# Kernel optimization log

Hardware: AMD Instinct MI355X
Metric: run time of the kernel (lower is better)

The kernel has to match this reference:

```python
import jax, jax.numpy as jnp
import numpy as np

TEMPERATURE = 0.05
BETA = 1.0
LAMBDA_THRESHOLD = 0.7


def setup_inputs() -> dict:
    key = jax.random.key(0)
    k1, k2 = jax.random.split(key)
    B, D = 8192, 256
    features = jax.random.normal(k1, (B, D), dtype=jnp.float32)
    labels = jax.random.randint(k2, (B,), 0, 100, dtype=jnp.int64)
    return {"features": features, "labels": labels}


def reference(features, labels):
    B = features.shape[0]
    eps = 1e-12
    # L2 normalize rows
    f = features / jnp.maximum(jnp.linalg.norm(features, axis=1, keepdims=True), eps)
    sim = jnp.matmul(f, f.T) / TEMPERATURE                      # [B, B]
    sim_max = jnp.max(sim, axis=1, keepdims=True)               # [B, 1]
    sim_stable = sim - sim_max

    same = (labels[:, None] == labels[None, :])
    eye = jnp.eye(B, dtype=bool)
    pos_mask = same & ~eye                                       # [B, B] bool

    # Denominator: logsumexp over all non-self entries per row
    exp_sim = jnp.exp(sim_stable) * (~eye)
    log_denom = jnp.log(jnp.sum(exp_sim, axis=1, keepdims=True) + eps) + sim_max  # [B,1]

    # SCL term: mean over positive pairs of (log_denom[i] - sim[i,j])
    pos_f = pos_mask.astype(sim.dtype)
    n_pos = jnp.sum(pos_f)
    scl_sum = jnp.sum(pos_f * (log_denom - sim))
    scl_loss = jnp.where(n_pos > 0, scl_sum / jnp.maximum(n_pos, 1.0), 0.0)

    # Relaxation term: per row, logsumexp over high-sim positive logits + baseline
    high = (sim * TEMPERATURE > LAMBDA_THRESHOLD) & pos_mask     # [B, B] bool
    neg_inf = jnp.asarray(-jnp.inf, sim.dtype)
    masked_logits = jnp.where(high, sim_stable, neg_inf)          # [B, B]
    baseline = (1.0 / TEMPERATURE) - sim_max                      # [B, 1]
    all_logits = jnp.concatenate([masked_logits, baseline], axis=1)  # [B, B+1]
    row_lse = jax.nn.logsumexp(all_logits, axis=1)                # [B]
    row_has = jnp.any(high, axis=1)
    n_high = jnp.sum(high.astype(sim.dtype))
    relax_sum = jnp.sum(jnp.where(row_has, row_lse, 0.0))
    relaxation_loss = jnp.where(n_high > 0, relax_sum / jnp.maximum(n_high, 1.0), 0.0)

    total = scl_loss + BETA * relaxation_loss
    return jnp.clip(total, 0.0, 10.0)
```

## Files before the change

### kernel.cpp

```cpp
#include <hip/hip_runtime.h>
#include <hip/hip_bf16.h>
#include <math.h>

#define B_N 8192
#define D_K 256
#define TILE 128
#define NT 512
#define NBLK 64
#define NPAIR 2080
#define NCLS 100
#define KEXP 28.8539008177792681f

typedef __attribute__((ext_vector_type(8))) short short8;
typedef __attribute__((ext_vector_type(4))) float f32x4;

__device__ __forceinline__ unsigned short f2bf(float x) {
    unsigned int u = __float_as_uint(x);
    unsigned int r = (u + 0x7FFFu + ((u >> 16) & 1u)) >> 16;
    return (unsigned short)r;
}

__device__ __forceinline__ void gload_lds16(const short* g, short* l) {
    __builtin_amdgcn_global_load_lds(
        (const __attribute__((address_space(1))) void*)g,
        (__attribute__((address_space(3))) void*)l, 16, 0, 0);
}

__global__ void prep_kernel(const float* __restrict__ feat, unsigned short* __restrict__ fnorm,
                            float* __restrict__ inv_norm, float* __restrict__ gscal) {
    if (blockIdx.x == 0 && threadIdx.x < 2) gscal[threadIdx.x] = 0.f;
    int wave = threadIdx.x >> 6, lane = threadIdx.x & 63;
    int row = blockIdx.x * 4 + wave;
    float4 v = *(const float4*)(feat + (size_t)row * D_K + lane * 4);
    float ss = v.x * v.x + v.y * v.y + v.z * v.z + v.w * v.w;
    #pragma unroll
    for (int off = 1; off < 64; off <<= 1) ss += __shfl_xor(ss, off);
    float inv = 1.0f / fmaxf(sqrtf(ss), 1e-12f);
    if (lane == 0) inv_norm[row] = inv;
    ushort4 o;
    o.x = f2bf(v.x * inv); o.y = f2bf(v.y * inv);
    o.z = f2bf(v.z * inv); o.w = f2bf(v.w * inv);
    *(ushort4*)(fnorm + (size_t)row * D_K + lane * 4) = o;
}

__global__ void hist_kernel(const float* __restrict__ feat, const int* __restrict__ labels,
                            const float* __restrict__ inv_norm,
                            int* __restrict__ cnt, float* __restrict__ gscal) {
    int c = blockIdx.x, tid = threadIdx.x;
    __shared__ unsigned short list[B_N];
    __shared__ int cntS;
    __shared__ float red[4];
    if (tid == 0) cntS = 0;
    __syncthreads();
    for (int r = tid; r < B_N; r += 256)
        if (labels[r] == c) { int p = atomicAdd(&cntS, 1); list[p] = (unsigned short)r; }
    __syncthreads();
    int n = cntS;
    float s = 0.f;
    #pragma unroll 8
    for (int k = 0; k < n; ++k) {
        int r = list[k];
        s += feat[(size_t)r * D_K + tid] * inv_norm[r];
    }
    float v = s * s;
    #pragma unroll
    for (int off = 1; off < 64; off <<= 1) v += __shfl_xor(v, off);
    if ((tid & 63) == 0) red[tid >> 6] = v;
    __syncthreads();
    if (tid == 0) {
        float tot = red[0] + red[1] + red[2] + red[3];
        cnt[c] = n;
        atomicAdd(&gscal[0], tot - (float)n);
    }
}

__global__ __launch_bounds__(NT, 4) void main_kernel(
        const unsigned short* __restrict__ fnorm, const int* __restrict__ labels,
        float2* __restrict__ G, float* __restrict__ gscal) {
    int bid = blockIdx.x;
    int b = (int)((sqrtf(8.0f * bid + 1.0f) - 1.0f) * 0.5f);
    while ((b + 1) * (b + 2) / 2 <= bid) ++b;
    while (b * (b + 1) / 2 > bid) --b;
    int a = bid - b * (b + 1) / 2;
    const int row0 = a * TILE, col0 = b * TILE;
    const bool diag = (a == b);

    __shared__ short As[TILE * 64];
    __shared__ short Bs[TILE * 64];
    __shared__ int Ls[2 * TILE];
    __shared__ int ghs[8];

    const int tid = threadIdx.x;
    const int lane = tid & 63, wave = tid >> 6;
    const int wm = wave >> 2, wn = wave & 3;
    const int l15 = lane & 15, lhi = lane >> 4;
    const short* fn = (const short*)fnorm;

    if (tid < 128) Ls[tid] = labels[row0 + tid];
    else if (tid < 256) Ls[tid] = labels[col0 + tid - 128];
    if (lane == 0) ghs[wave] = 0;

    f32x4 acc[4][2];
    #pragma unroll
    for (int i = 0; i < 4; i++)
        #pragma unroll
        for (int j = 0; j < 2; j++) acc[i][j] = {0.f, 0.f, 0.f, 0.f};

    for (int kc = 0; kc < 4; ++kc) {
        #pragma unroll
        for (int li = 0; li < 2; ++li) {
            int id = tid + li * NT;
            int r = id >> 3, c = id & 7;
            int cs = c ^ (r & 7);
            int ub = (id & ~63) * 8;
            gload_lds16(fn + (size_t)(row0 + r) * D_K + kc * 64 + cs * 8, &As[ub]);
            gload_lds16(fn + (size_t)(col0 + r) * D_K + kc * 64 + cs * 8, &Bs[ub]);
        }
        __syncthreads();
        #pragma unroll
        for (int ks = 0; ks < 2; ++ks) {
            short8 af[4], bfr[2];
            #pragma unroll
            for (int mi = 0; mi < 4; mi++) {
                int row = wm * 64 + mi * 16 + l15;
                int ch = (ks * 4 + lhi) ^ (l15 & 7);
                af[mi] = *(const short8*)&As[row * 64 + ch * 8];
            }
            #pragma unroll
            for (int ni = 0; ni < 2; ni++) {
                int row = wn * 32 + ni * 16 + l15;
                int ch = (ks * 4 + lhi) ^ (l15 & 7);
                bfr[ni] = *(const short8*)&Bs[row * 64 + ch * 8];
            }
            #pragma unroll
            for (int mi = 0; mi < 4; mi++)
                #pragma unroll
                for (int ni = 0; ni < 2; ni++)
                    acc[mi][ni] = __builtin_amdgcn_mfma_f32_16x16x32_bf16(af[mi], bfr[ni], acc[mi][ni], 0, 0, 0);
        }
        __syncthreads();
    }

    float2* Rbuf = (float2*)As;
    float2* Cbuf = (float2*)Bs;

    int lc[2], colg[2];
    #pragma unroll
    for (int ni = 0; ni < 2; ni++) {
        int c = wn * 32 + ni * 16 + l15;
        lc[ni] = Ls[128 + c];
        colg[ni] = col0 + c;
    }

    float cD[2] = {0.f, 0.f};
    unsigned int hmask = 0;

    #pragma unroll
    for (int mi = 0; mi < 4; mi++) {
        #pragma unroll
        for (int reg = 0; reg < 4; reg++) {
            int rloc = wm * 64 + mi * 16 + lhi * 4 + reg;
            int rowg = row0 + rloc;
            int lr = Ls[rloc];
            float d = 0.f;
            #pragma unroll
            for (int ni = 0; ni < 2; ni++) {
                float dot = acc[mi][ni][reg];
                float e = __builtin_exp2f((dot - 1.0f) * KEXP);
                bool ns = (rowg != colg[ni]);
                float ev = ns ? e : 0.f;
                d += ev; cD[ni] += ev;
                bool hi = ns && (lr == lc[ni]) && (dot > 0.7f);
                hmask |= hi ? (1u << ((mi * 4 + reg) * 2 + ni)) : 0u;
            }
            #pragma unroll
            for (int off = 1; off < 16; off <<= 1) d += __shfl_xor(d, off);
            if (l15 == 0) Rbuf[wn * 128 + rloc] = {d, 0.f};
        }
    }

    if (!diag) {
        #pragma unroll
        for (int ni = 0; ni < 2; ni++) {
            #pragma unroll
            for (int off = 16; off < 64; off <<= 1) cD[ni] += __shfl_xor(cD[ni], off);
        }
        if (lhi == 0) {
            #pragma unroll
            for (int ni = 0; ni < 2; ni++)
                Cbuf[wm * 128 + wn * 32 + ni * 16 + l15] = {cD[ni], 0.f};
        }
    }

    if (__any(hmask != 0)) {
        float cR[2] = {0.f, 0.f};
        #pragma unroll
        for (int mi = 0; mi < 4; mi++) {
            #pragma unroll
            for (int reg = 0; reg < 4; reg++) {
                int rloc = wm * 64 + mi * 16 + lhi * 4 + reg;
                float rx = 0.f;
                #pragma unroll
                for (int ni = 0; ni < 2; ni++) {
                    if (hmask & (1u << ((mi * 4 + reg) * 2 + ni))) {
                        float e = __builtin_exp2f((acc[mi][ni][reg] - 1.0f) * KEXP);
                        rx += e; cR[ni] += e;
                    }
                }
                #pragma unroll
                for (int off = 1; off < 16; off <<= 1) rx += __shfl_xor(rx, off);
                if (l15 == 0) Rbuf[wn * 128 + rloc].y = rx;
            }
        }
        if (!diag) {
            #pragma unroll
            for (int ni = 0; ni < 2; ni++) {
                #pragma unroll
                for (int off = 16; off < 64; off <<= 1) cR[ni] += __shfl_xor(cR[ni], off);
            }
            if (lhi == 0) {
                #pragma unroll
                for (int ni = 0; ni < 2; ni++)
                    Cbuf[wm * 128 + wn * 32 + ni * 16 + l15].y = cR[ni];
            }
        }
        int nhi = __popc(hmask);
        #pragma unroll
        for (int off = 1; off < 64; off <<= 1) nhi += __shfl_xor(nhi, off);
        if (lane == 0) ghs[wave] = nhi;
    }
    __syncthreads();

    if (tid < 128) {
        int r = tid;
        float2 a0 = Rbuf[r], a1 = Rbuf[128 + r], a2 = Rbuf[256 + r], a3 = Rbuf[384 + r];
        G[(size_t)b * B_N + row0 + r] = {a0.x + a1.x + a2.x + a3.x, a0.y + a1.y + a2.y + a3.y};
    } else if (tid < 256 && !diag) {
        int c = tid - 128;
        float2 a0 = Cbuf[c], a1 = Cbuf[128 + c];
        G[(size_t)a * B_N + col0 + c] = {a0.x + a1.x, a0.y + a1.y};
    }
    if (tid == 0) {
        int tot = ghs[0] + ghs[1] + ghs[2] + ghs[3] + ghs[4] + ghs[5] + ghs[6] + ghs[7];
        if (tot > 0) {
            float w = diag ? 1.0f : 2.0f;
            atomicAdd(&gscal[1], w * (float)tot);
        }
    }
}

__global__ void finalize1(const float2* __restrict__ G, const int* __restrict__ labels,
                          const int* __restrict__ cnt, double* __restrict__ part) {
    int lane = threadIdx.x & 63, q = threadIdx.x >> 6;
    int r = blockIdx.x * 64 + lane;
    float d = 0.f, rx = 0.f;
    #pragma unroll
    for (int s = 0; s < 16; ++s) {
        float2 g = G[(size_t)(q * 16 + s) * B_N + r];
        d += g.x; rx += g.y;
    }
    __shared__ float2 sh[4][64];
    sh[q][lane] = {d, rx};
    __syncthreads();
    if (threadIdx.x < 64) {
        int rr = blockIdx.x * 64 + threadIdx.x;
        float2 t0 = sh[0][threadIdx.x], t1 = sh[1][threadIdx.x];
        float2 t2 = sh[2][threadIdx.x], t3 = sh[3][threadIdx.x];
        float dd = t0.x + t1.x + t2.x + t3.x;
        float rr2 = t0.y + t1.y + t2.y + t3.y;
        float np = (float)(cnt[labels[rr]] - 1);
        float ld = logf(dd + 1e-12f) + 20.0f;
        double s1 = (double)np * (double)ld;
        double s2 = (double)np;
        double s3 = (rr2 > 0.f) ? (double)logf(rr2 + 1.0f) : 0.0;
        #pragma unroll
        for (int off = 1; off < 64; off <<= 1) {
            s1 += __shfl_xor(s1, off);
            s2 += __shfl_xor(s2, off);
            s3 += __shfl_xor(s3, off);
        }
        if (threadIdx.x == 0) {
            part[blockIdx.x * 3 + 0] = s1;
            part[blockIdx.x * 3 + 1] = s2;
            part[blockIdx.x * 3 + 2] = s3;
        }
    }
}

__global__ void finalize2(const double* __restrict__ part, const float* __restrict__ gscal,
                          float* __restrict__ out) {
    int t = threadIdx.x;
    double s1 = part[t * 3 + 0], s2 = part[t * 3 + 1], s3 = part[t * 3 + 2];
    #pragma unroll
    for (int off = 1; off < 64; off <<= 1) {
        s1 += __shfl_xor(s1, off);
        s2 += __shfl_xor(s2, off);
        s3 += __shfl_xor(s3, off);
    }
    __shared__ double sh[2][3];
    int wave = t >> 6, lane = t & 63;
    if (lane == 0) { sh[wave][0] = s1; sh[wave][1] = s2; sh[wave][2] = s3; }
    __syncthreads();
    if (t == 0) {
        double a1 = sh[0][0] + sh[1][0];
        double a2 = sh[0][1] + sh[1][1];
        double a3 = sh[0][2] + sh[1][2];
        double gp = (double)gscal[0];
        double gh = (double)gscal[1];
        double scl = (a2 > 0.0) ? (a1 - 20.0 * gp) / fmax(a2, 1.0) : 0.0;
        double rel = (gh > 0.0) ? a3 / fmax(gh, 1.0) : 0.0;
        double tot = scl + rel;
        tot = fmin(fmax(tot, 0.0), 10.0);
        out[0] = (float)tot;
    }
}

extern "C" void kernel_launch(void* const* d_in, const int* in_sizes, int n_in,
                              void* d_out, int out_size, void* d_ws, size_t ws_size,
                              hipStream_t stream) {
    const float* feat = (const float*)d_in[0];
    const int* labels = (const int*)d_in[1];
    float* out = (float*)d_out;
    char* ws = (char*)d_ws;

    unsigned short* fnorm = (unsigned short*)(ws);
    float2* G        = (float2*)(ws + (size_t)4 * 1024 * 1024);
    float*  inv_norm = (float*)(ws + (size_t)8 * 1024 * 1024);
    double* part     = (double*)(ws + (size_t)8 * 1024 * 1024 + 32768);
    float*  gscal    = (float*)(ws + (size_t)8 * 1024 * 1024 + 36864);
    int*    cnt      = (int*)(ws + (size_t)8 * 1024 * 1024 + 40960);

    prep_kernel<<<B_N / 4, 256, 0, stream>>>(feat, fnorm, inv_norm, gscal);
    hist_kernel<<<NCLS, 256, 0, stream>>>(feat, labels, inv_norm, cnt, gscal);
    main_kernel<<<NPAIR, NT, 0, stream>>>(fnorm, labels, G, gscal);
    finalize1<<<B_N / 64, 256, 0, stream>>>(G, labels, cnt, part);
    finalize2<<<1, 128, 0, stream>>>(part, gscal, out);
    (void)in_sizes; (void)n_in; (void)out_size; (void)ws_size;
}
```

Baseline: 128.7 us.

## Fold class histogram into prep and main kernels, merge finalize stages

Removes the separate hist_kernel. Label counts are now built in block 0 of prep_kernel, and the sum of positive-pair dot products is accumulated inside main_kernel's epilogue instead of through per-class feature sums. finalize1 and finalize2 are merged into one kernel that uses double atomics and a last-block-done counter. Launch bounds on main_kernel are raised to request more resident blocks. This cuts two kernel launches and the serial hist pass, but adds per-tile reductions and atomics, and the positive sum is now computed from bf16 dot products rather than fp32 features.

```diff
diff --git a/kernel.cpp b/kernel.cpp
--- a/kernel.cpp
+++ b/kernel.cpp
@@ -27,8 +27,23 @@
 }
 
 __global__ void prep_kernel(const float* __restrict__ feat, unsigned short* __restrict__ fnorm,
-                            float* __restrict__ inv_norm, float* __restrict__ gscal) {
-    if (blockIdx.x == 0 && threadIdx.x < 2) gscal[threadIdx.x] = 0.f;
+                            const int* __restrict__ labels, int* __restrict__ cnt,
+                            float* __restrict__ gscal, double* __restrict__ accum,
+                            unsigned int* __restrict__ done) {
+    if (blockIdx.x == 0) {
+        __shared__ int h[NCLS];
+        int t = threadIdx.x;
+        if (t < NCLS) h[t] = 0;
+        if (t == 0) {
+            gscal[0] = 0.f; gscal[1] = 0.f;
+            accum[0] = 0.0; accum[1] = 0.0; accum[2] = 0.0;
+            *done = 0u;
+        }
+        __syncthreads();
+        for (int r = t; r < B_N; r += 256) atomicAdd(&h[labels[r]], 1);
+        __syncthreads();
+        if (t < NCLS) cnt[t] = h[t];
+    }
     int wave = threadIdx.x >> 6, lane = threadIdx.x & 63;
     int row = blockIdx.x * 4 + wave;
     float4 v = *(const float4*)(feat + (size_t)row * D_K + lane * 4);
@@ -36,45 +51,13 @@
     #pragma unroll
     for (int off = 1; off < 64; off <<= 1) ss += __shfl_xor(ss, off);
     float inv = 1.0f / fmaxf(sqrtf(ss), 1e-12f);
-    if (lane == 0) inv_norm[row] = inv;
     ushort4 o;
     o.x = f2bf(v.x * inv); o.y = f2bf(v.y * inv);
     o.z = f2bf(v.z * inv); o.w = f2bf(v.w * inv);
     *(ushort4*)(fnorm + (size_t)row * D_K + lane * 4) = o;
 }
 
-__global__ void hist_kernel(const float* __restrict__ feat, const int* __restrict__ labels,
-                            const float* __restrict__ inv_norm,
-                            int* __restrict__ cnt, float* __restrict__ gscal) {
-    int c = blockIdx.x, tid = threadIdx.x;
-    __shared__ unsigned short list[B_N];
-    __shared__ int cntS;
-    __shared__ float red[4];
-    if (tid == 0) cntS = 0;
-    __syncthreads();
-    for (int r = tid; r < B_N; r += 256)
-        if (labels[r] == c) { int p = atomicAdd(&cntS, 1); list[p] = (unsigned short)r; }
-    __syncthreads();
-    int n = cntS;
-    float s = 0.f;
-    #pragma unroll 8
-    for (int k = 0; k < n; ++k) {
-        int r = list[k];
-        s += feat[(size_t)r * D_K + tid] * inv_norm[r];
-    }
-    float v = s * s;
-    #pragma unroll
-    for (int off = 1; off < 64; off <<= 1) v += __shfl_xor(v, off);
-    if ((tid & 63) == 0) red[tid >> 6] = v;
-    __syncthreads();
-    if (tid == 0) {
-        float tot = red[0] + red[1] + red[2] + red[3];
-        cnt[c] = n;
-        atomicAdd(&gscal[0], tot - (float)n);
-    }
-}
-
-__global__ __launch_bounds__(NT, 4) void main_kernel(
+__global__ __launch_bounds__(NT, 8) void main_kernel(
         const unsigned short* __restrict__ fnorm, const int* __restrict__ labels,
         float2* __restrict__ G, float* __restrict__ gscal) {
     int bid = blockIdx.x;
@@ -89,6 +72,7 @@
     __shared__ short Bs[TILE * 64];
     __shared__ int Ls[2 * TILE];
     __shared__ int ghs[8];
+    __shared__ float gps[8];
 
     const int tid = threadIdx.x;
     const int lane = tid & 63, wave = tid >> 6;
@@ -153,6 +137,7 @@
     }
 
     float cD[2] = {0.f, 0.f};
+    float gp = 0.f;
     unsigned int hmask = 0;
 
     #pragma unroll
@@ -170,7 +155,9 @@
                 bool ns = (rowg != colg[ni]);
                 float ev = ns ? e : 0.f;
                 d += ev; cD[ni] += ev;
-                bool hi = ns && (lr == lc[ni]) && (dot > 0.7f);
+                bool ps = ns && (lr == lc[ni]);
+                gp += ps ? dot : 0.f;
+                bool hi = ps && (dot > 0.7f);
                 hmask |= hi ? (1u << ((mi * 4 + reg) * 2 + ni)) : 0u;
             }
             #pragma unroll
@@ -191,6 +178,10 @@
                 Cbuf[wm * 128 + wn * 32 + ni * 16 + l15] = {cD[ni], 0.f};
         }
     }
+
+    #pragma unroll
+    for (int off = 1; off < 64; off <<= 1) gp += __shfl_xor(gp, off);
+    if (lane == 0) gps[wave] = gp;
 
     if (__any(hmask != 0)) {
         float cR[2] = {0.f, 0.f};
@@ -241,16 +232,18 @@
         G[(size_t)a * B_N + col0 + c] = {a0.x + a1.x, a0.y + a1.y};
     }
     if (tid == 0) {
+        float w = diag ? 1.0f : 2.0f;
+        float gpt = gps[0] + gps[1] + gps[2] + gps[3] + gps[4] + gps[5] + gps[6] + gps[7];
+        atomicAdd(&gscal[0], w * gpt);
         int tot = ghs[0] + ghs[1] + ghs[2] + ghs[3] + ghs[4] + ghs[5] + ghs[6] + ghs[7];
-        if (tot > 0) {
-            float w = diag ? 1.0f : 2.0f;
-            atomicAdd(&gscal[1], w * (float)tot);
-        }
-    }
-}
-
-__global__ void finalize1(const float2* __restrict__ G, const int* __restrict__ labels,
-                          const int* __restrict__ cnt, double* __restrict__ part) {
+        if (tot > 0) atomicAdd(&gscal[1], w * (float)tot);
+    }
+}
+
+__global__ void finalize_kernel(const float2* __restrict__ G, const int* __restrict__ labels,
+                                const int* __restrict__ cnt, const float* __restrict__ gscal,
+                                double* __restrict__ accum, unsigned int* __restrict__ done,
+                                float* __restrict__ out) {
     int lane = threadIdx.x & 63, q = threadIdx.x >> 6;
     int r = blockIdx.x * 64 + lane;
     float d = 0.f, rx = 0.f;
@@ -280,38 +273,24 @@
             s3 += __shfl_xor(s3, off);
         }
         if (threadIdx.x == 0) {
-            part[blockIdx.x * 3 + 0] = s1;
-            part[blockIdx.x * 3 + 1] = s2;
-            part[blockIdx.x * 3 + 2] = s3;
-        }
-    }
-}
-
-__global__ void finalize2(const double* __restrict__ part, const float* __restrict__ gscal,
-                          float* __restrict__ out) {
-    int t = threadIdx.x;
-    double s1 = part[t * 3 + 0], s2 = part[t * 3 + 1], s3 = part[t * 3 + 2];
-    #pragma unroll
-    for (int off = 1; off < 64; off <<= 1) {
-        s1 += __shfl_xor(s1, off);
-        s2 += __shfl_xor(s2, off);
-        s3 += __shfl_xor(s3, off);
-    }
-    __shared__ double sh[2][3];
-    int wave = t >> 6, lane = t & 63;
-    if (lane == 0) { sh[wave][0] = s1; sh[wave][1] = s2; sh[wave][2] = s3; }
-    __syncthreads();
-    if (t == 0) {
-        double a1 = sh[0][0] + sh[1][0];
-        double a2 = sh[0][1] + sh[1][1];
-        double a3 = sh[0][2] + sh[1][2];
-        double gp = (double)gscal[0];
-        double gh = (double)gscal[1];
-        double scl = (a2 > 0.0) ? (a1 - 20.0 * gp) / fmax(a2, 1.0) : 0.0;
-        double rel = (gh > 0.0) ? a3 / fmax(gh, 1.0) : 0.0;
-        double tot = scl + rel;
-        tot = fmin(fmax(tot, 0.0), 10.0);
-        out[0] = (float)tot;
+            atomicAdd(&accum[0], s1);
+            atomicAdd(&accum[1], s2);
+            atomicAdd(&accum[2], s3);
+            __threadfence();
+            unsigned int tk = atomicAdd(done, 1u);
+            if (tk == gridDim.x - 1) {
+                double a1 = atomicAdd(&accum[0], 0.0);
+                double a2 = atomicAdd(&accum[1], 0.0);
+                double a3 = atomicAdd(&accum[2], 0.0);
+                double gp = (double)gscal[0];
+                double gh = (double)gscal[1];
+                double scl = (a2 > 0.0) ? (a1 - 20.0 * gp) / fmax(a2, 1.0) : 0.0;
+                double rel = (gh > 0.0) ? a3 / fmax(gh, 1.0) : 0.0;
+                double tot = scl + rel;
+                tot = fmin(fmax(tot, 0.0), 10.0);
+                out[0] = (float)tot;
+            }
+        }
     }
 }
 
@@ -324,16 +303,14 @@
     char* ws = (char*)d_ws;
 
     unsigned short* fnorm = (unsigned short*)(ws);
-    float2* G        = (float2*)(ws + (size_t)4 * 1024 * 1024);
-    float*  inv_norm = (float*)(ws + (size_t)8 * 1024 * 1024);
-    double* part     = (double*)(ws + (size_t)8 * 1024 * 1024 + 32768);
-    float*  gscal    = (float*)(ws + (size_t)8 * 1024 * 1024 + 36864);
-    int*    cnt      = (int*)(ws + (size_t)8 * 1024 * 1024 + 40960);
-
-    prep_kernel<<<B_N / 4, 256, 0, stream>>>(feat, fnorm, inv_norm, gscal);
-    hist_kernel<<<NCLS, 256, 0, stream>>>(feat, labels, inv_norm, cnt, gscal);
+    float2* G          = (float2*)(ws + (size_t)4 * 1024 * 1024);
+    int*    cnt        = (int*)(ws + (size_t)8 * 1024 * 1024);
+    float*  gscal      = (float*)(ws + (size_t)8 * 1024 * 1024 + 1024);
+    double* accum      = (double*)(ws + (size_t)8 * 1024 * 1024 + 2048);
+    unsigned int* done = (unsigned int*)(ws + (size_t)8 * 1024 * 1024 + 3072);
+
+    prep_kernel<<<B_N / 4, 256, 0, stream>>>(feat, fnorm, labels, cnt, gscal, accum, done);
     main_kernel<<<NPAIR, NT, 0, stream>>>(fnorm, labels, G, gscal);
-    finalize1<<<B_N / 64, 256, 0, stream>>>(G, labels, cnt, part);
-    finalize2<<<1, 128, 0, stream>>>(part, gscal, out);
+    finalize_kernel<<<B_N / 64, 256, 0, stream>>>(G, labels, cnt, gscal, accum, done, out);
     (void)in_sizes; (void)n_in; (void)out_size; (void)ws_size;
 }
```

After: 162.1 us. 26.0% more time.
